# Optimization experiments

Hardware: AMD Instinct MI355X
Metric: run time of the kernel (lower is better)

Reference implementation:

```python
import jax, jax.numpy as jnp
import numpy as np

N_NODES = 50000
N_EDGES = 800000
IN_CH = 256
H1, D1 = 4, 64   # layer 1: 4 heads x 64 -> 256
H2, D2 = 1, 64   # output layer: 1 head x 64
NEG_SLOPE = 0.2  # DGL GATConv default


def _leaky_relu(x):
    return jnp.where(x >= 0, x, NEG_SLOPE * x)


def gat_conv(h, src, dst, W, attn_l, attn_r, bias, res_W, num_heads, out_feats, apply_elu):
    """DGL GATConv (eval mode, feat_drop=attn_drop=0).
    h: (N, F_in); src/dst: (E,) edge endpoints (edge u->v aggregates at v).
    W: (F_in, H*D); attn_l/attn_r: (H, D); bias: (H*D,); res_W: (F_in, H*D) or None.
    Returns (N, H, D).
    """
    N = h.shape[0]
    ft = (h @ W).reshape(N, num_heads, out_feats)            # (N,H,D)
    el = jnp.sum(ft * attn_l, axis=-1)                        # (N,H)
    er = jnp.sum(ft * attn_r, axis=-1)                        # (N,H)
    e = _leaky_relu(el[src] + er[dst])                        # (E,H)
    # segment softmax over incoming edges of each dst node
    emax = jax.ops.segment_max(e, dst, num_segments=N)        # (N,H)
    emax = jax.lax.stop_gradient(emax)
    ee = jnp.exp(e - emax[dst])                               # (E,H)
    denom = jax.ops.segment_sum(ee, dst, num_segments=N)      # (N,H)
    a = ee / denom[dst]                                       # (E,H)
    msg = ft[src] * a[:, :, None]                             # (E,H,D)
    rst = jax.ops.segment_sum(msg, dst, num_segments=N)       # (N,H,D)
    if res_W is not None:
        rst = rst + (h @ res_W).reshape(N, num_heads, out_feats)
    rst = rst + bias.reshape(num_heads, out_feats)
    if apply_elu:
        rst = jax.nn.elu(rst)
    return rst


def setup_inputs() -> dict:
    key = jax.random.key(0)
    ks = jax.random.split(key, 12)
    feat = jax.random.normal(ks[0], (N_NODES, IN_CH), dtype=jnp.float32)
    src = jax.random.randint(ks[1], (N_EDGES,), 0, N_NODES)
    dst = jax.random.randint(ks[2], (N_EDGES,), 0, N_NODES)
    s = 0.1
    W1 = jax.random.normal(ks[3], (IN_CH, H1 * D1), dtype=jnp.float32) * s
    al1 = jax.random.normal(ks[4], (H1, D1), dtype=jnp.float32) * s
    ar1 = jax.random.normal(ks[5], (H1, D1), dtype=jnp.float32) * s
    b1 = jnp.zeros((H1 * D1,), dtype=jnp.float32)
    W2 = jax.random.normal(ks[6], (H1 * D1, H2 * D2), dtype=jnp.float32) * s
    al2 = jax.random.normal(ks[7], (H2, D2), dtype=jnp.float32) * s
    ar2 = jax.random.normal(ks[8], (H2, D2), dtype=jnp.float32) * s
    b2 = jnp.zeros((H2 * D2,), dtype=jnp.float32)
    resW2 = jax.random.normal(ks[9], (H1 * D1, H2 * D2), dtype=jnp.float32) * s
    return {"feat": feat, "src": src, "dst": dst,
            "W1": W1, "al1": al1, "ar1": ar1, "b1": b1,
            "W2": W2, "al2": al2, "ar2": ar2, "b2": b2, "resW2": resW2}


def reference(feat, src, dst, W1, al1, ar1, b1, W2, al2, ar2, b2, resW2):
    # Layer 1: 4 heads, ELU, no residual (first DGL layer built without residual)
    h = gat_conv(feat, src, dst, W1, al1, ar1, b1, None, H1, D1, True)
    h = h.reshape(N_NODES, H1 * D1)  # flatten(1)
    # Layer 2: 1 head, residual (linear res_fc since 256 != 64), no activation
    h = gat_conv(h, src, dst, W2, al2, ar2, b2, resW2, H2, D2, False)
    return h.mean(axis=1)  # mean over output heads -> (N, out_channels)
```

## Files before the change

kernel.cpp:

```cpp
#include <hip/hip_runtime.h>
#include <math.h>

#define N_NODES 50000
#define N_EDGES 800000
#define ELL_W 64
#define CNT_STRIDE 16

#define E_SPLIT 400000
#define CONV_BLKS 1024
#define SCAT_BLKS 1024

typedef __attribute__((ext_vector_type(8))) short bf16x8;
typedef __attribute__((ext_vector_type(4))) float f32x4;
typedef __attribute__((ext_vector_type(2))) float f32x2;

__device__ __forceinline__ float leaky(float x) { return x >= 0.f ? x : 0.2f * x; }
__device__ __forceinline__ unsigned short f2bf(float f) {
  unsigned u = __float_as_uint(f);
  return (unsigned short)((u + 0x7fffu + ((u >> 16) & 1u)) >> 16);
}
__device__ __forceinline__ float bflo(unsigned u) { return __uint_as_float(u << 16); }
__device__ __forceinline__ float bfhi(unsigned u) { return __uint_as_float(u & 0xffff0000u); }
__device__ __forceinline__ unsigned pack2(float a, float b) {
  return (unsigned)f2bf(a) | ((unsigned)f2bf(b) << 16);
}

__device__ __forceinline__ void scat4(const int* __restrict__ src, const int* __restrict__ dst,
                                      int* __restrict__ cnt, unsigned short* __restrict__ ell,
                                      int e) {
  int4 d4 = *(const int4*)(dst + e);
  int4 s4 = *(const int4*)(src + e);
  int sl;
  sl = atomicAdd(cnt + d4.x * CNT_STRIDE, 1);
  if (sl < ELL_W) __builtin_nontemporal_store((unsigned short)s4.x, ell + d4.x * ELL_W + sl);
  sl = atomicAdd(cnt + d4.y * CNT_STRIDE, 1);
  if (sl < ELL_W) __builtin_nontemporal_store((unsigned short)s4.y, ell + d4.y * ELL_W + sl);
  sl = atomicAdd(cnt + d4.z * CNT_STRIDE, 1);
  if (sl < ELL_W) __builtin_nontemporal_store((unsigned short)s4.z, ell + d4.z * ELL_W + sl);
  sl = atomicAdd(cnt + d4.w * CNT_STRIDE, 1);
  if (sl < ELL_W) __builtin_nontemporal_store((unsigned short)s4.w, ell + d4.w * ELL_W + sl);
}

__launch_bounds__(256)
__global__ void prep_k(const float* __restrict__ feat, const float* __restrict__ W1,
                       const float* __restrict__ W2, const float* __restrict__ resW2,
                       short* __restrict__ featb, short* __restrict__ Wt1,
                       short* __restrict__ Wt2, const int* __restrict__ src,
                       const int* __restrict__ dst, int* __restrict__ cnt,
                       unsigned short* __restrict__ ell) {
  if (blockIdx.x < SCAT_BLKS) {
    const int gtid = blockIdx.x * 256 + threadIdx.x;
    const int gsz = SCAT_BLKS * 256;
    for (int q = gtid; q < E_SPLIT / 4; q += gsz) scat4(src, dst, cnt, ell, q * 4);
    return;
  }
  const int gtid = (blockIdx.x - SCAT_BLKS) * 256 + threadIdx.x;
  const int gsz = CONV_BLKS * 256;
  for (int idx = gtid; idx < 256 * 256; idx += gsz) {
    int n = idx >> 8, k = idx & 255;
    Wt1[idx] = (short)f2bf(W1[(size_t)k * 256 + n]);
  }
  for (int idx = gtid; idx < 128 * 256; idx += gsz) {
    int n = idx >> 8, k = idx & 255;
    float v = (n < 64) ? W2[(size_t)k * 64 + n] : resW2[(size_t)k * 64 + (n - 64)];
    Wt2[idx] = (short)f2bf(v);
  }
  const float4* f4 = (const float4*)feat;
  uint2* fb2 = (uint2*)featb;
  for (int idx = gtid; idx < N_NODES * 64; idx += gsz) {
    float4 f = f4[idx];
    uint2 o;
    o.x = pack2(f.x, f.y);
    o.y = pack2(f.z, f.w);
    fb2[idx] = o;
  }
}

template <int MODE, bool SCAT>
__launch_bounds__(256)
__global__ void mfma_gemm_k(const short* __restrict__ A, const short* __restrict__ Bt,
                            const float* __restrict__ bias, const float* __restrict__ al,
                            const float* __restrict__ ar, float* __restrict__ elp,
                            float* __restrict__ erp, short* __restrict__ Cb,
                            float* __restrict__ Cf, const int* __restrict__ src,
                            const int* __restrict__ dst, int* __restrict__ cnt,
                            unsigned short* __restrict__ ell, int M, int K, int N) {
  constexpr int EPI_COLS = (MODE == 0) ? 136 : 72;
  union SharedU {
    struct { short As[4][128][8]; short Bs[4][128][8]; } ab;
    short epi[128 * EPI_COLS];
  };
  __shared__ SharedU sh;

  if (SCAT && blockIdx.y < 2) {
    const int gtid = (blockIdx.y * gridDim.x + blockIdx.x) * 256 + threadIdx.x;
    if (gtid < (N_EDGES - E_SPLIT) / 4) scat4(src, dst, cnt, ell, E_SPLIT + gtid * 4);
    return;
  }
  const int tid = threadIdx.x;
  const int bm0 = blockIdx.x * 128;
  const int bn0 = (SCAT ? ((int)blockIdx.y - 2) : (int)blockIdx.y) * 128;
  const int wave = tid >> 6, lane = tid & 63;
  const int wm = (wave & 1) * 64, wn = (wave >> 1) * 64;
  const int q = lane >> 4, r16 = lane & 15;
  const int srow = tid >> 1, sk = (tid & 1) * 16, sq = (tid & 1) * 2;
  f32x4 acc[4][4] = {};

  for (int k0 = 0; k0 < K; k0 += 32) {
    {
      uint4 v0 = {0, 0, 0, 0}, v1 = {0, 0, 0, 0};
      if (bm0 + srow < M) {
        const uint4* p = (const uint4*)(A + (size_t)(bm0 + srow) * K + k0 + sk);
        v0 = p[0];
        v1 = p[1];
      }
      *(uint4*)&sh.ab.As[sq][srow][0] = v0;
      *(uint4*)&sh.ab.As[sq + 1][srow][0] = v1;
    }
    {
      const uint4* p = (const uint4*)(Bt + (size_t)(bn0 + srow) * K + k0 + sk);
      *(uint4*)&sh.ab.Bs[sq][srow][0] = p[0];
      *(uint4*)&sh.ab.Bs[sq + 1][srow][0] = p[1];
    }
    __syncthreads();
    bf16x8 af[4], bfr[4];
#pragma unroll
    for (int i = 0; i < 4; ++i) af[i] = *(const bf16x8*)&sh.ab.As[q][wm + i * 16 + r16][0];
#pragma unroll
    for (int j = 0; j < 4; ++j) bfr[j] = *(const bf16x8*)&sh.ab.Bs[q][wn + j * 16 + r16][0];
#pragma unroll
    for (int i = 0; i < 4; ++i)
#pragma unroll
      for (int j = 0; j < 4; ++j)
        acc[i][j] = __builtin_amdgcn_mfma_f32_16x16x32_bf16(af[i], bfr[j], acc[i][j], 0, 0, 0);
    __syncthreads();
  }

  if (MODE == 0 || wn == 0) {
    const int head = (bn0 + wn) >> 6;
    float alv[4], arv[4];
#pragma unroll
    for (int j = 0; j < 4; ++j) {
      alv[j] = al[((MODE == 0) ? head * 64 : 0) + j * 16 + r16];
      arv[j] = ar[((MODE == 0) ? head * 64 : 0) + j * 16 + r16];
    }
#pragma unroll
    for (int i = 0; i < 4; ++i) {
#pragma unroll
      for (int reg = 0; reg < 4; ++reg) {
        float dl = acc[i][0][reg] * alv[0] + acc[i][1][reg] * alv[1] +
                   acc[i][2][reg] * alv[2] + acc[i][3][reg] * alv[3];
        float dr = acc[i][0][reg] * arv[0] + acc[i][1][reg] * arv[1] +
                   acc[i][2][reg] * arv[2] + acc[i][3][reg] * arv[3];
#pragma unroll
        for (int mm = 1; mm < 16; mm <<= 1) {
          dl += __shfl_xor(dl, mm);
          dr += __shfl_xor(dr, mm);
        }
        int row_g = bm0 + wm + i * 16 + q * 4 + reg;
        if (r16 == 0 && row_g < M) {
          if (MODE == 0) {
            elp[(size_t)row_g * 4 + head] = dl;
            erp[(size_t)row_g * 4 + head] = dr;
          } else {
            elp[row_g] = dl;
            erp[row_g] = dr;
          }
        }
      }
    }
  }

  if (MODE == 0) {
#pragma unroll
    for (int i = 0; i < 4; ++i)
#pragma unroll
      for (int reg = 0; reg < 4; ++reg) {
        int row = wm + i * 16 + q * 4 + reg;
#pragma unroll
        for (int j = 0; j < 4; ++j)
          sh.epi[row * EPI_COLS + wn + j * 16 + r16] = (short)f2bf(acc[i][j][reg]);
      }
    __syncthreads();
#pragma unroll
    for (int k = 0; k < 8; ++k) {
      int c = k * 256 + tid;
      int row = c >> 4, cc = c & 15;
      int row_g = bm0 + row;
      if (row_g < M) {
        uint4 v = *(const uint4*)&sh.epi[row * EPI_COLS + cc * 8];
        *(uint4*)(Cb + (size_t)row_g * N + bn0 + cc * 8) = v;
      }
    }
  } else {
    if (wn == 0) {
#pragma unroll
      for (int i = 0; i < 4; ++i)
#pragma unroll
        for (int reg = 0; reg < 4; ++reg) {
          int row = wm + i * 16 + q * 4 + reg;
#pragma unroll
          for (int j = 0; j < 4; ++j)
            sh.epi[row * EPI_COLS + j * 16 + r16] = (short)f2bf(acc[i][j][reg]);
        }
    } else {
#pragma unroll
      for (int i = 0; i < 4; ++i)
#pragma unroll
        for (int reg = 0; reg < 4; ++reg) {
          int row_g = bm0 + wm + i * 16 + q * 4 + reg;
          if (row_g >= M) continue;
#pragma unroll
          for (int j = 0; j < 4; ++j) {
            int col = j * 16 + r16;
            Cf[(size_t)row_g * 64 + col] = acc[i][j][reg] + bias[col];
          }
        }
    }
    __syncthreads();
#pragma unroll
    for (int k = 0; k < 4; ++k) {
      int c = k * 256 + tid;
      int row = c >> 3, cc = c & 7;
      int row_g = bm0 + row;
      if (row_g < M) {
        uint4 v = *(const uint4*)&sh.epi[row * EPI_COLS + cc * 8];
        *(uint4*)(Cb + (size_t)row_g * 64 + cc * 8) = v;
      }
    }
  }
}

#define AGG1_FMA(ACC, U, W)                     \
  {                                             \
    f32x2 w2_ = {(W), (W)};                     \
    ACC[0] += w2_ * (f32x2){bflo((U).x), bfhi((U).x)}; \
    ACC[1] += w2_ * (f32x2){bflo((U).y), bfhi((U).y)}; \
    ACC[2] += w2_ * (f32x2){bflo((U).z), bfhi((U).z)}; \
    ACC[3] += w2_ * (f32x2){bflo((U).w), bfhi((U).w)}; \
  }

__launch_bounds__(256)
__global__ void agg1_k(const unsigned short* __restrict__ ell, const int* __restrict__ cnt,
                       const float* __restrict__ el, const float* __restrict__ er,
                       const short* __restrict__ ft, const float* __restrict__ bias,
                       short* __restrict__ h1) {
  __shared__ uint2 wmeta[4][2][64][4];
  const int wv = threadIdx.x >> 6;
  const int lane = threadIdx.x & 63;
  const int nodeA = blockIdx.x * 8 + wv * 2;
  const int nodeB = nodeA + 1;
  const int degA = min(cnt[nodeA * CNT_STRIDE], ELL_W);
  const int degB = min(cnt[nodeB * CNT_STRIDE], ELL_W);
  const unsigned short* rowA = ell + nodeA * ELL_W;
  const unsigned short* rowB = ell + nodeB * ELL_W;

  {
    int sA = lane < degA ? (int)rowA[lane] : (degA > 0 ? (int)rowA[0] : 0);
    int sB = lane < degB ? (int)rowB[lane] : (degB > 0 ? (int)rowB[0] : 0);
    float4 elA = *(const float4*)(el + (size_t)sA * 4);
    float4 elB = *(const float4*)(el + (size_t)sB * 4);
    float4 erA = *(const float4*)(er + (size_t)nodeA * 4);
    float4 erB = *(const float4*)(er + (size_t)nodeB * 4);
    float a0 = lane < degA ? __expf(leaky(elA.x + erA.x)) : 0.f;
    float a1 = lane < degA ? __expf(leaky(elA.y + erA.y)) : 0.f;
    float a2 = lane < degA ? __expf(leaky(elA.z + erA.z)) : 0.f;
    float a3 = lane < degA ? __expf(leaky(elA.w + erA.w)) : 0.f;
    float b0 = lane < degB ? __expf(leaky(elB.x + erB.x)) : 0.f;
    float b1 = lane < degB ? __expf(leaky(elB.y + erB.y)) : 0.f;
    float b2 = lane < degB ? __expf(leaky(elB.z + erB.z)) : 0.f;
    float b3 = lane < degB ? __expf(leaky(elB.w + erB.w)) : 0.f;
    float dA0 = a0, dA1 = a1, dA2 = a2, dA3 = a3;
    float dB0 = b0, dB1 = b1, dB2 = b2, dB3 = b3;
#pragma unroll
    for (int m = 1; m < 64; m <<= 1) {
      dA0 += __shfl_xor(dA0, m);
      dB0 += __shfl_xor(dB0, m);
      dA1 += __shfl_xor(dA1, m);
      dB1 += __shfl_xor(dB1, m);
      dA2 += __shfl_xor(dA2, m);
      dB2 += __shfl_xor(dB2, m);
      dA3 += __shfl_xor(dA3, m);
      dB3 += __shfl_xor(dB3, m);
    }
    unsigned ofA = (unsigned)sA * 512u, ofB = (unsigned)sB * 512u;
    uint4 pa0, pa1, pb0, pb1;
    pa0.x = ofA; pa0.y = __float_as_uint(degA > 0 ? a0 / dA0 : 0.f);
    pa0.z = ofA; pa0.w = __float_as_uint(degA > 0 ? a1 / dA1 : 0.f);
    pa1.x = ofA; pa1.y = __float_as_uint(degA > 0 ? a2 / dA2 : 0.f);
    pa1.z = ofA; pa1.w = __float_as_uint(degA > 0 ? a3 / dA3 : 0.f);
    pb0.x = ofB; pb0.y = __float_as_uint(degB > 0 ? b0 / dB0 : 0.f);
    pb0.z = ofB; pb0.w = __float_as_uint(degB > 0 ? b1 / dB1 : 0.f);
    pb1.x = ofB; pb1.y = __float_as_uint(degB > 0 ? b2 / dB2 : 0.f);
    pb1.z = ofB; pb1.w = __float_as_uint(degB > 0 ? b3 / dB3 : 0.f);
    *(uint4*)&wmeta[wv][0][lane][0] = pa0;
    *(uint4*)&wmeta[wv][0][lane][2] = pa1;
    *(uint4*)&wmeta[wv][1][lane][0] = pb0;
    *(uint4*)&wmeta[wv][1][lane][2] = pb1;
  }

  const int half = lane >> 5, l5 = lane & 31, h = l5 >> 3;
  const char* ftb = (const char*)ft + l5 * 16;
  f32x2 accA[4] = {}, accB[4] = {};
  const int degM = max((degA + 7) & ~7, (degB + 7) & ~7);
  for (int i = 0; i < degM; i += 8) {
    unsigned oA[4], oB[4];
    float wA[4], wB[4];
#pragma unroll
    for (int k = 0; k < 4; ++k) {
      uint2 mA = wmeta[wv][0][i + k * 2 + half][h];
      uint2 mB = wmeta[wv][1][i + k * 2 + half][h];
      oA[k] = mA.x;
      wA[k] = __uint_as_float(mA.y);
      oB[k] = mB.x;
      wB[k] = __uint_as_float(mB.y);
    }
    uint4 uA[4], uB[4];
#pragma unroll
    for (int k = 0; k < 4; ++k) {
      uA[k] = *(const uint4*)(ftb + oA[k]);
      uB[k] = *(const uint4*)(ftb + oB[k]);
    }
#pragma unroll
    for (int k = 0; k < 4; ++k) {
      AGG1_FMA(accA, uA[k], wA[k]);
      AGG1_FMA(accB, uB[k], wB[k]);
    }
  }

#pragma unroll
  for (int j = 0; j < 4; ++j) {
    accA[j][0] += __shfl_xor(accA[j][0], 32);
    accA[j][1] += __shfl_xor(accA[j][1], 32);
    accB[j][0] += __shfl_xor(accB[j][0], 32);
    accB[j][1] += __shfl_xor(accB[j][1], 32);
  }
  const int node = half ? nodeB : nodeA;
  float v[8];
#pragma unroll
  for (int j = 0; j < 4; ++j) {
    v[2 * j] = half ? accB[j][0] : accA[j][0];
    v[2 * j + 1] = half ? accB[j][1] : accA[j][1];
  }
  float4 b0 = *(const float4*)(bias + l5 * 8);
  float4 b1 = *(const float4*)(bias + l5 * 8 + 4);
  v[0] += b0.x; v[1] += b0.y; v[2] += b0.z; v[3] += b0.w;
  v[4] += b1.x; v[5] += b1.y; v[6] += b1.z; v[7] += b1.w;
#pragma unroll
  for (int k = 0; k < 8; ++k) v[k] = v[k] > 0.f ? v[k] : expm1f(v[k]);
  uint4 o;
  o.x = pack2(v[0], v[1]);
  o.y = pack2(v[2], v[3]);
  o.z = pack2(v[4], v[5]);
  o.w = pack2(v[6], v[7]);
  *(uint4*)(h1 + (size_t)node * 256 + l5 * 8) = o;
}

__launch_bounds__(256)
__global__ void agg2_k(const unsigned short* __restrict__ ell, const int* __restrict__ cnt,
                       const float* __restrict__ el, const float* __restrict__ er,
                       const short* __restrict__ ft, float* __restrict__ out) {
  __shared__ uint2 wsl[4][2][64];
  const int wv = threadIdx.x >> 6;
  const int lane = threadIdx.x & 63;
  const int nodeA = blockIdx.x * 8 + wv * 2;
  const int nodeB = nodeA + 1;
  const int degA = min(cnt[nodeA * CNT_STRIDE], ELL_W);
  const int degB = min(cnt[nodeB * CNT_STRIDE], ELL_W);
  const unsigned short* rowA = ell + nodeA * ELL_W;
  const unsigned short* rowB = ell + nodeB * ELL_W;

  {
    int sA = lane < degA ? (int)rowA[lane] : (degA > 0 ? (int)rowA[0] : 0);
    int sB = lane < degB ? (int)rowB[lane] : (degB > 0 ? (int)rowB[0] : 0);
    float wa = lane < degA ? __expf(leaky(el[sA] + er[nodeA])) : 0.f;
    float wb = lane < degB ? __expf(leaky(el[sB] + er[nodeB])) : 0.f;
    float da = wa, db = wb;
#pragma unroll
    for (int m = 1; m < 64; m <<= 1) {
      da += __shfl_xor(da, m);
      db += __shfl_xor(db, m);
    }
    uint2 ea, eb;
    ea.x = (unsigned)sA * 128u;
    ea.y = __float_as_uint(degA > 0 ? wa / da : 0.f);
    eb.x = (unsigned)sB * 128u;
    eb.y = __float_as_uint(degB > 0 ? wb / db : 0.f);
    wsl[wv][0][lane] = ea;
    wsl[wv][1][lane] = eb;
  }

  const int qtr = lane >> 4, l4 = lane & 15;
  const char* ftb = (const char*)ft + l4 * 8;
  f32x2 accA[2] = {}, accB[2] = {};
  const int degM = max((degA + 7) & ~7, (degB + 7) & ~7);
  for (int i = 0; i < degM; i += 8) {
#pragma unroll
    for (int k = 0; k < 2; ++k) {
      int slot = i + k * 4 + qtr;
      uint2 ea = wsl[wv][0][slot];
      uint2 eb = wsl[wv][1][slot];
      uint2 ua = *(const uint2*)(ftb + ea.x);
      uint2 ub = *(const uint2*)(ftb + eb.x);
      float wa = __uint_as_float(ea.y);
      float wb = __uint_as_float(eb.y);
      f32x2 wa2 = {wa, wa}, wb2 = {wb, wb};
      accA[0] += wa2 * (f32x2){bflo(ua.x), bfhi(ua.x)};
      accA[1] += wa2 * (f32x2){bflo(ua.y), bfhi(ua.y)};
      accB[0] += wb2 * (f32x2){bflo(ub.x), bfhi(ub.x)};
      accB[1] += wb2 * (f32x2){bflo(ub.y), bfhi(ub.y)};
    }
  }
#pragma unroll
  for (int j = 0; j < 2; ++j) {
#pragma unroll
    for (int c = 0; c < 2; ++c) {
      accA[j][c] += __shfl_xor(accA[j][c], 16);
      accA[j][c] += __shfl_xor(accA[j][c], 32);
      accB[j][c] += __shfl_xor(accB[j][c], 16);
      accB[j][c] += __shfl_xor(accB[j][c], 32);
    }
  }
  if (lane < 32) {
    const int node = lane < 16 ? nodeA : nodeB;
    float4 add;
    add.x = lane < 16 ? accA[0][0] : accB[0][0];
    add.y = lane < 16 ? accA[0][1] : accB[0][1];
    add.z = lane < 16 ? accA[1][0] : accB[1][0];
    add.w = lane < 16 ? accA[1][1] : accB[1][1];
    float4* po = (float4*)(out + (size_t)node * 64 + l4 * 4);
    float4 o = *po;
    o.x += add.x;
    o.y += add.y;
    o.z += add.z;
    o.w += add.w;
    *po = o;
  }
}

extern "C" void kernel_launch(void* const* d_in, const int* in_sizes, int n_in,
                              void* d_out, int out_size, void* d_ws, size_t ws_size,
                              hipStream_t stream) {
  const float* feat  = (const float*)d_in[0];
  const int*   src   = (const int*)d_in[1];
  const int*   dst   = (const int*)d_in[2];
  const float* W1    = (const float*)d_in[3];
  const float* al1   = (const float*)d_in[4];
  const float* ar1   = (const float*)d_in[5];
  const float* b1    = (const float*)d_in[6];
  const float* W2    = (const float*)d_in[7];
  const float* al2   = (const float*)d_in[8];
  const float* ar2   = (const float*)d_in[9];
  const float* b2    = (const float*)d_in[10];
  const float* resW2 = (const float*)d_in[11];
  float* out = (float*)d_out;

  char* p = (char*)d_ws;
  short* featb = (short*)p; p += (size_t)N_NODES * 256 * 2;
  short* ft1b = (short*)p; p += (size_t)N_NODES * 256 * 2;
  short* h1b  = (short*)p; p += (size_t)N_NODES * 256 * 2;
  short* ft2b = (short*)p; p += (size_t)N_NODES * 64 * 2;
  short* Wt1  = (short*)p; p += 256 * 256 * 2;
  short* Wt2  = (short*)p; p += 128 * 256 * 2;
  float* el1  = (float*)p; p += (size_t)N_NODES * 4 * 4;
  float* er1  = (float*)p; p += (size_t)N_NODES * 4 * 4;
  float* el2  = (float*)p; p += (size_t)N_NODES * 4;
  float* er2  = (float*)p; p += (size_t)N_NODES * 4;
  int* cnt    = (int*)p;   p += (size_t)N_NODES * CNT_STRIDE * 4;
  unsigned short* ell = (unsigned short*)p; p += (size_t)N_NODES * ELL_W * 2;

  hipMemsetAsync(cnt, 0, (size_t)N_NODES * CNT_STRIDE * sizeof(int), stream);

  dim3 blk(256);

  prep_k<<<SCAT_BLKS + CONV_BLKS, blk, 0, stream>>>(feat, W1, W2, resW2, featb, Wt1, Wt2,
                                                    src, dst, cnt, ell);

  mfma_gemm_k<0, true><<<dim3(391, 4), blk, 0, stream>>>(
      featb, Wt1, nullptr, al1, ar1, el1, er1, ft1b, nullptr,
      src, dst, cnt, ell, N_NODES, 256, 256);
  agg1_k<<<6250, blk, 0, stream>>>(ell, cnt, el1, er1, ft1b, b1, h1b);

  mfma_gemm_k<1, false><<<dim3(391, 1), blk, 0, stream>>>(
      h1b, Wt2, b2, al2, ar2, el2, er2, ft2b, out,
      nullptr, nullptr, nullptr, nullptr, N_NODES, 256, 128);
  agg2_k<<<6250, blk, 0, stream>>>(ell, cnt, el2, er2, ft2b, out);
}
```

Before: 274.4 us.

## Split layer-1 aggregation into per-head column slices across 8x more blocks

The layer-1 aggregation kernel now launches eight blocks per node group. Each block handles one 32-column slice of a single head, so per-lane work drops from 16-byte loads covering all four heads to 8-byte loads within one head. This cuts register and shared-memory use per block and raises parallelism and occupancy for the gather. The cost is that the attention softmax, the ELL index reads and the el/er loads are recomputed in each of the eight slices, with narrower, less efficient memory transactions.

```diff
diff --git a/kernel.cpp b/kernel.cpp
--- a/kernel.cpp
+++ b/kernel.cpp
@@ -231,25 +231,19 @@
   }
 }
 
-#define AGG1_FMA(ACC, U, W)                     \
-  {                                             \
-    f32x2 w2_ = {(W), (W)};                     \
-    ACC[0] += w2_ * (f32x2){bflo((U).x), bfhi((U).x)}; \
-    ACC[1] += w2_ * (f32x2){bflo((U).y), bfhi((U).y)}; \
-    ACC[2] += w2_ * (f32x2){bflo((U).z), bfhi((U).z)}; \
-    ACC[3] += w2_ * (f32x2){bflo((U).w), bfhi((U).w)}; \
-  }
-
 __launch_bounds__(256)
 __global__ void agg1_k(const unsigned short* __restrict__ ell, const int* __restrict__ cnt,
                        const float* __restrict__ el, const float* __restrict__ er,
                        const short* __restrict__ ft, const float* __restrict__ bias,
                        short* __restrict__ h1) {
-  __shared__ uint2 wmeta[4][2][64][4];
+  __shared__ uint2 wsl[4][2][64];
+  const int slice = blockIdx.x & 7;
+  const int grp = blockIdx.x >> 3;
+  const int head = slice >> 1;
+  const unsigned coff = (unsigned)(head * 128 + (slice & 1) * 64);
   const int wv = threadIdx.x >> 6;
   const int lane = threadIdx.x & 63;
-  const int nodeA = blockIdx.x * 8 + wv * 2;
-  const int nodeB = nodeA + 1;
+  const int nodeA = grp * 8 + wv * 2, nodeB = nodeA + 1;
   const int degA = min(cnt[nodeA * CNT_STRIDE], ELL_W);
   const int degB = min(cnt[nodeB * CNT_STRIDE], ELL_W);
   const unsigned short* rowA = ell + nodeA * ELL_W;
@@ -258,102 +252,58 @@
   {
     int sA = lane < degA ? (int)rowA[lane] : (degA > 0 ? (int)rowA[0] : 0);
     int sB = lane < degB ? (int)rowB[lane] : (degB > 0 ? (int)rowB[0] : 0);
-    float4 elA = *(const float4*)(el + (size_t)sA * 4);
-    float4 elB = *(const float4*)(el + (size_t)sB * 4);
-    float4 erA = *(const float4*)(er + (size_t)nodeA * 4);
-    float4 erB = *(const float4*)(er + (size_t)nodeB * 4);
-    float a0 = lane < degA ? __expf(leaky(elA.x + erA.x)) : 0.f;
-    float a1 = lane < degA ? __expf(leaky(elA.y + erA.y)) : 0.f;
-    float a2 = lane < degA ? __expf(leaky(elA.z + erA.z)) : 0.f;
-    float a3 = lane < degA ? __expf(leaky(elA.w + erA.w)) : 0.f;
-    float b0 = lane < degB ? __expf(leaky(elB.x + erB.x)) : 0.f;
-    float b1 = lane < degB ? __expf(leaky(elB.y + erB.y)) : 0.f;
-    float b2 = lane < degB ? __expf(leaky(elB.z + erB.z)) : 0.f;
-    float b3 = lane < degB ? __expf(leaky(elB.w + erB.w)) : 0.f;
-    float dA0 = a0, dA1 = a1, dA2 = a2, dA3 = a3;
-    float dB0 = b0, dB1 = b1, dB2 = b2, dB3 = b3;
+    float wa = lane < degA ? __expf(leaky(el[sA * 4 + head] + er[nodeA * 4 + head])) : 0.f;
+    float wb = lane < degB ? __expf(leaky(el[sB * 4 + head] + er[nodeB * 4 + head])) : 0.f;
+    float da = wa, db = wb;
 #pragma unroll
     for (int m = 1; m < 64; m <<= 1) {
-      dA0 += __shfl_xor(dA0, m);
-      dB0 += __shfl_xor(dB0, m);
-      dA1 += __shfl_xor(dA1, m);
-      dB1 += __shfl_xor(dB1, m);
-      dA2 += __shfl_xor(dA2, m);
-      dB2 += __shfl_xor(dB2, m);
-      dA3 += __shfl_xor(dA3, m);
-      dB3 += __shfl_xor(dB3, m);
-    }
-    unsigned ofA = (unsigned)sA * 512u, ofB = (unsigned)sB * 512u;
-    uint4 pa0, pa1, pb0, pb1;
-    pa0.x = ofA; pa0.y = __float_as_uint(degA > 0 ? a0 / dA0 : 0.f);
-    pa0.z = ofA; pa0.w = __float_as_uint(degA > 0 ? a1 / dA1 : 0.f);
-    pa1.x = ofA; pa1.y = __float_as_uint(degA > 0 ? a2 / dA2 : 0.f);
-    pa1.z = ofA; pa1.w = __float_as_uint(degA > 0 ? a3 / dA3 : 0.f);
-    pb0.x = ofB; pb0.y = __float_as_uint(degB > 0 ? b0 / dB0 : 0.f);
-    pb0.z = ofB; pb0.w = __float_as_uint(degB > 0 ? b1 / dB1 : 0.f);
-    pb1.x = ofB; pb1.y = __float_as_uint(degB > 0 ? b2 / dB2 : 0.f);
-    pb1.z = ofB; pb1.w = __float_as_uint(degB > 0 ? b3 / dB3 : 0.f);
-    *(uint4*)&wmeta[wv][0][lane][0] = pa0;
-    *(uint4*)&wmeta[wv][0][lane][2] = pa1;
-    *(uint4*)&wmeta[wv][1][lane][0] = pb0;
-    *(uint4*)&wmeta[wv][1][lane][2] = pb1;
-  }
-
-  const int half = lane >> 5, l5 = lane & 31, h = l5 >> 3;
-  const char* ftb = (const char*)ft + l5 * 16;
-  f32x2 accA[4] = {}, accB[4] = {};
-  const int degM = max((degA + 7) & ~7, (degB + 7) & ~7);
-  for (int i = 0; i < degM; i += 8) {
-    unsigned oA[4], oB[4];
-    float wA[4], wB[4];
-#pragma unroll
-    for (int k = 0; k < 4; ++k) {
-      uint2 mA = wmeta[wv][0][i + k * 2 + half][h];
-      uint2 mB = wmeta[wv][1][i + k * 2 + half][h];
-      oA[k] = mA.x;
-      wA[k] = __uint_as_float(mA.y);
-      oB[k] = mB.x;
-      wB[k] = __uint_as_float(mB.y);
-    }
-    uint4 uA[4], uB[4];
-#pragma unroll
-    for (int k = 0; k < 4; ++k) {
-      uA[k] = *(const uint4*)(ftb + oA[k]);
-      uB[k] = *(const uint4*)(ftb + oB[k]);
-    }
-#pragma unroll
-    for (int k = 0; k < 4; ++k) {
-      AGG1_FMA(accA, uA[k], wA[k]);
-      AGG1_FMA(accB, uB[k], wB[k]);
-    }
-  }
-
-#pragma unroll
-  for (int j = 0; j < 4; ++j) {
-    accA[j][0] += __shfl_xor(accA[j][0], 32);
-    accA[j][1] += __shfl_xor(accA[j][1], 32);
-    accB[j][0] += __shfl_xor(accB[j][0], 32);
-    accB[j][1] += __shfl_xor(accB[j][1], 32);
-  }
-  const int node = half ? nodeB : nodeA;
-  float v[8];
-#pragma unroll
-  for (int j = 0; j < 4; ++j) {
-    v[2 * j] = half ? accB[j][0] : accA[j][0];
-    v[2 * j + 1] = half ? accB[j][1] : accA[j][1];
-  }
-  float4 b0 = *(const float4*)(bias + l5 * 8);
-  float4 b1 = *(const float4*)(bias + l5 * 8 + 4);
-  v[0] += b0.x; v[1] += b0.y; v[2] += b0.z; v[3] += b0.w;
-  v[4] += b1.x; v[5] += b1.y; v[6] += b1.z; v[7] += b1.w;
-#pragma unroll
-  for (int k = 0; k < 8; ++k) v[k] = v[k] > 0.f ? v[k] : expm1f(v[k]);
-  uint4 o;
-  o.x = pack2(v[0], v[1]);
-  o.y = pack2(v[2], v[3]);
-  o.z = pack2(v[4], v[5]);
-  o.w = pack2(v[6], v[7]);
-  *(uint4*)(h1 + (size_t)node * 256 + l5 * 8) = o;
+      da += __shfl_xor(da, m);
+      db += __shfl_xor(db, m);
+    }
+    uint2 ea, eb;
+    ea.x = (unsigned)sA * 512u + coff;
+    ea.y = __float_as_uint(degA > 0 ? wa / da : 0.f);
+    eb.x = (unsigned)sB * 512u + coff;
+    eb.y = __float_as_uint(degB > 0 ? wb / db : 0.f);
+    wsl[wv][0][lane] = ea;
+    wsl[wv][1][lane] = eb;
+  }
+
+  const int half = lane >> 5, l5 = lane & 31;
+  const int eg = l5 >> 3, li = l5 & 7;
+  const char* ftb = (const char*)ft + li * 8;
+  f32x2 acc0 = {}, acc1 = {};
+  const int degM = max((degA + 3) & ~3, (degB + 3) & ~3);
+  for (int i = 0; i < degM; i += 4) {
+    uint2 m = wsl[wv][half][i + eg];
+    uint2 u = *(const uint2*)(ftb + m.x);
+    float w = __uint_as_float(m.y);
+    f32x2 w2 = {w, w};
+    acc0 += w2 * (f32x2){bflo(u.x), bfhi(u.x)};
+    acc1 += w2 * (f32x2){bflo(u.y), bfhi(u.y)};
+  }
+  acc0[0] += __shfl_xor(acc0[0], 8);
+  acc0[1] += __shfl_xor(acc0[1], 8);
+  acc1[0] += __shfl_xor(acc1[0], 8);
+  acc1[1] += __shfl_xor(acc1[1], 8);
+  acc0[0] += __shfl_xor(acc0[0], 16);
+  acc0[1] += __shfl_xor(acc0[1], 16);
+  acc1[0] += __shfl_xor(acc1[0], 16);
+  acc1[1] += __shfl_xor(acc1[1], 16);
+  if (eg == 0) {
+    const int node = half ? nodeB : nodeA;
+    const float* bp = bias + head * 64 + (slice & 1) * 32 + li * 4;
+    float4 b = *(const float4*)bp;
+    float v0 = acc0[0] + b.x, v1 = acc0[1] + b.y, v2 = acc1[0] + b.z, v3 = acc1[1] + b.w;
+    v0 = v0 > 0.f ? v0 : expm1f(v0);
+    v1 = v1 > 0.f ? v1 : expm1f(v1);
+    v2 = v2 > 0.f ? v2 : expm1f(v2);
+    v3 = v3 > 0.f ? v3 : expm1f(v3);
+    uint2 o;
+    o.x = pack2(v0, v1);
+    o.y = pack2(v2, v3);
+    *(uint2*)((char*)h1 + (size_t)node * 512 + coff + li * 8) = o;
+  }
 }
 
 __launch_bounds__(256)
@@ -479,7 +429,7 @@
   mfma_gemm_k<0, true><<<dim3(391, 4), blk, 0, stream>>>(
       featb, Wt1, nullptr, al1, ar1, el1, er1, ft1b, nullptr,
       src, dst, cnt, ell, N_NODES, 256, 256);
-  agg1_k<<<6250, blk, 0, stream>>>(ell, cnt, el1, er1, ft1b, b1, h1b);
+  agg1_k<<<50000, blk, 0, stream>>>(ell, cnt, el1, er1, ft1b, b1, h1b);
 
   mfma_gemm_k<1, false><<<dim3(391, 1), blk, 0, stream>>>(
       h1b, Wt2, b2, al2, ar2, el2, er2, ft2b, out,
```

Result: slower. 361.5 us (+31.7%).

## Build ELL adjacency with per-block node ranges and LDS atomic counters

Applied to the files above, without the earlier changes.

Replaces the global-atomic edge scatter, which was split between prep and the first GEMM, with 128 blocks that each own a contiguous range of 391 destination nodes. Each block scans the whole dst array and counts its nodes' edges with shared-memory atomics. It then writes the counts densely, which removes the padded count array and the memset. Each block rereads all 800K dst indices, so total reads are about 128 times higher and the build runs on only 128 blocks, which could lengthen prep's critical path.

```diff
diff --git a/kernel.cpp b/kernel.cpp
--- a/kernel.cpp
+++ b/kernel.cpp
@@ -4,11 +4,10 @@
 #define N_NODES 50000
 #define N_EDGES 800000
 #define ELL_W 64
-#define CNT_STRIDE 16
-
-#define E_SPLIT 400000
+
+#define BLD_BLKS 128
+#define BLD_RANGE 391
 #define CONV_BLKS 1024
-#define SCAT_BLKS 1024
 
 typedef __attribute__((ext_vector_type(8))) short bf16x8;
 typedef __attribute__((ext_vector_type(4))) float f32x4;
@@ -23,22 +22,6 @@
 __device__ __forceinline__ float bfhi(unsigned u) { return __uint_as_float(u & 0xffff0000u); }
 __device__ __forceinline__ unsigned pack2(float a, float b) {
   return (unsigned)f2bf(a) | ((unsigned)f2bf(b) << 16);
-}
-
-__device__ __forceinline__ void scat4(const int* __restrict__ src, const int* __restrict__ dst,
-                                      int* __restrict__ cnt, unsigned short* __restrict__ ell,
-                                      int e) {
-  int4 d4 = *(const int4*)(dst + e);
-  int4 s4 = *(const int4*)(src + e);
-  int sl;
-  sl = atomicAdd(cnt + d4.x * CNT_STRIDE, 1);
-  if (sl < ELL_W) __builtin_nontemporal_store((unsigned short)s4.x, ell + d4.x * ELL_W + sl);
-  sl = atomicAdd(cnt + d4.y * CNT_STRIDE, 1);
-  if (sl < ELL_W) __builtin_nontemporal_store((unsigned short)s4.y, ell + d4.y * ELL_W + sl);
-  sl = atomicAdd(cnt + d4.z * CNT_STRIDE, 1);
-  if (sl < ELL_W) __builtin_nontemporal_store((unsigned short)s4.z, ell + d4.z * ELL_W + sl);
-  sl = atomicAdd(cnt + d4.w * CNT_STRIDE, 1);
-  if (sl < ELL_W) __builtin_nontemporal_store((unsigned short)s4.w, ell + d4.w * ELL_W + sl);
 }
 
 __launch_bounds__(256)
@@ -48,13 +31,41 @@
                        short* __restrict__ Wt2, const int* __restrict__ src,
                        const int* __restrict__ dst, int* __restrict__ cnt,
                        unsigned short* __restrict__ ell) {
-  if (blockIdx.x < SCAT_BLKS) {
-    const int gtid = blockIdx.x * 256 + threadIdx.x;
-    const int gsz = SCAT_BLKS * 256;
-    for (int q = gtid; q < E_SPLIT / 4; q += gsz) scat4(src, dst, cnt, ell, q * 4);
+  __shared__ int cnt_l[BLD_RANGE];
+  if (blockIdx.x < BLD_BLKS) {
+    const int base = blockIdx.x * BLD_RANGE;
+    const int nloc = min(BLD_RANGE, N_NODES - base);
+    for (int i = threadIdx.x; i < BLD_RANGE; i += 256) cnt_l[i] = 0;
+    __syncthreads();
+    const int4* d4p = (const int4*)dst;
+    for (int q = threadIdx.x; q < N_EDGES / 4; q += 256) {
+      int4 d4 = d4p[q];
+      unsigned r0 = (unsigned)(d4.x - base);
+      unsigned r1 = (unsigned)(d4.y - base);
+      unsigned r2 = (unsigned)(d4.z - base);
+      unsigned r3 = (unsigned)(d4.w - base);
+      if (r0 < (unsigned)nloc) {
+        int sl = atomicAdd(&cnt_l[r0], 1);
+        if (sl < ELL_W) ell[(size_t)d4.x * ELL_W + sl] = (unsigned short)src[q * 4 + 0];
+      }
+      if (r1 < (unsigned)nloc) {
+        int sl = atomicAdd(&cnt_l[r1], 1);
+        if (sl < ELL_W) ell[(size_t)d4.y * ELL_W + sl] = (unsigned short)src[q * 4 + 1];
+      }
+      if (r2 < (unsigned)nloc) {
+        int sl = atomicAdd(&cnt_l[r2], 1);
+        if (sl < ELL_W) ell[(size_t)d4.z * ELL_W + sl] = (unsigned short)src[q * 4 + 2];
+      }
+      if (r3 < (unsigned)nloc) {
+        int sl = atomicAdd(&cnt_l[r3], 1);
+        if (sl < ELL_W) ell[(size_t)d4.w * ELL_W + sl] = (unsigned short)src[q * 4 + 3];
+      }
+    }
+    __syncthreads();
+    for (int i = threadIdx.x; i < nloc; i += 256) cnt[base + i] = cnt_l[i];
     return;
   }
-  const int gtid = (blockIdx.x - SCAT_BLKS) * 256 + threadIdx.x;
+  const int gtid = (blockIdx.x - BLD_BLKS) * 256 + threadIdx.x;
   const int gsz = CONV_BLKS * 256;
   for (int idx = gtid; idx < 256 * 256; idx += gsz) {
     int n = idx >> 8, k = idx & 255;
@@ -76,15 +87,13 @@
   }
 }
 
-template <int MODE, bool SCAT>
+template <int MODE>
 __launch_bounds__(256)
 __global__ void mfma_gemm_k(const short* __restrict__ A, const short* __restrict__ Bt,
                             const float* __restrict__ bias, const float* __restrict__ al,
                             const float* __restrict__ ar, float* __restrict__ elp,
                             float* __restrict__ erp, short* __restrict__ Cb,
-                            float* __restrict__ Cf, const int* __restrict__ src,
-                            const int* __restrict__ dst, int* __restrict__ cnt,
-                            unsigned short* __restrict__ ell, int M, int K, int N) {
+                            float* __restrict__ Cf, int M, int K, int N) {
   constexpr int EPI_COLS = (MODE == 0) ? 136 : 72;
   union SharedU {
     struct { short As[4][128][8]; short Bs[4][128][8]; } ab;
@@ -92,14 +101,9 @@
   };
   __shared__ SharedU sh;
 
-  if (SCAT && blockIdx.y < 2) {
-    const int gtid = (blockIdx.y * gridDim.x + blockIdx.x) * 256 + threadIdx.x;
-    if (gtid < (N_EDGES - E_SPLIT) / 4) scat4(src, dst, cnt, ell, E_SPLIT + gtid * 4);
-    return;
-  }
   const int tid = threadIdx.x;
   const int bm0 = blockIdx.x * 128;
-  const int bn0 = (SCAT ? ((int)blockIdx.y - 2) : (int)blockIdx.y) * 128;
+  const int bn0 = blockIdx.y * 128;
   const int wave = tid >> 6, lane = tid & 63;
   const int wm = (wave & 1) * 64, wn = (wave >> 1) * 64;
   const int q = lane >> 4, r16 = lane & 15;
@@ -250,8 +254,8 @@
   const int lane = threadIdx.x & 63;
   const int nodeA = blockIdx.x * 8 + wv * 2;
   const int nodeB = nodeA + 1;
-  const int degA = min(cnt[nodeA * CNT_STRIDE], ELL_W);
-  const int degB = min(cnt[nodeB * CNT_STRIDE], ELL_W);
+  const int degA = min(cnt[nodeA], ELL_W);
+  const int degB = min(cnt[nodeB], ELL_W);
   const unsigned short* rowA = ell + nodeA * ELL_W;
   const unsigned short* rowB = ell + nodeB * ELL_W;
 
@@ -365,8 +369,8 @@
   const int lane = threadIdx.x & 63;
   const int nodeA = blockIdx.x * 8 + wv * 2;
   const int nodeB = nodeA + 1;
-  const int degA = min(cnt[nodeA * CNT_STRIDE], ELL_W);
-  const int degB = min(cnt[nodeB * CNT_STRIDE], ELL_W);
+  const int degA = min(cnt[nodeA], ELL_W);
+  const int degB = min(cnt[nodeB], ELL_W);
   const unsigned short* rowA = ell + nodeA * ELL_W;
   const unsigned short* rowB = ell + nodeB * ELL_W;
 
@@ -466,23 +470,19 @@
   float* er1  = (float*)p; p += (size_t)N_NODES * 4 * 4;
   float* el2  = (float*)p; p += (size_t)N_NODES * 4;
   float* er2  = (float*)p; p += (size_t)N_NODES * 4;
-  int* cnt    = (int*)p;   p += (size_t)N_NODES * CNT_STRIDE * 4;
+  int* cnt    = (int*)p;   p += (size_t)N_NODES * 4;
   unsigned short* ell = (unsigned short*)p; p += (size_t)N_NODES * ELL_W * 2;
 
-  hipMemsetAsync(cnt, 0, (size_t)N_NODES * CNT_STRIDE * sizeof(int), stream);
-
   dim3 blk(256);
 
-  prep_k<<<SCAT_BLKS + CONV_BLKS, blk, 0, stream>>>(feat, W1, W2, resW2, featb, Wt1, Wt2,
-                                                    src, dst, cnt, ell);
-
-  mfma_gemm_k<0, true><<<dim3(391, 4), blk, 0, stream>>>(
-      featb, Wt1, nullptr, al1, ar1, el1, er1, ft1b, nullptr,
-      src, dst, cnt, ell, N_NODES, 256, 256);
+  prep_k<<<BLD_BLKS + CONV_BLKS, blk, 0, stream>>>(feat, W1, W2, resW2, featb, Wt1, Wt2,
+                                                   src, dst, cnt, ell);
+
+  mfma_gemm_k<0><<<dim3(391, 2), blk, 0, stream>>>(
+      featb, Wt1, nullptr, al1, ar1, el1, er1, ft1b, nullptr, N_NODES, 256, 256);
   agg1_k<<<6250, blk, 0, stream>>>(ell, cnt, el1, er1, ft1b, b1, h1b);
 
-  mfma_gemm_k<1, false><<<dim3(391, 1), blk, 0, stream>>>(
-      h1b, Wt2, b2, al2, ar2, el2, er2, ft2b, out,
-      nullptr, nullptr, nullptr, nullptr, N_NODES, 256, 128);
+  mfma_gemm_k<1><<<dim3(391, 1), blk, 0, stream>>>(
+      h1b, Wt2, b2, al2, ar2, el2, er2, ft2b, out, N_NODES, 256, 128);
   agg2_k<<<6250, blk, 0, stream>>>(ell, cnt, el2, er2, ft2b, out);
 }
```

Result: slower. 676.7 us (+146.6%).
